# Kernel tuning notes

Measured on AMD Instinct MI355X. Metric: run time of the kernel, lower is better.

## Reference

```python
import jax, jax.numpy as jnp
import numpy as np

EPS = 1e-5
K_NBR = 21   # num_neighbors + 1 (self)
PSI = 4


def _bn(x, g, b):
    # BatchNorm (training-mode forward): channel-last, normalize over all other axes
    axes = tuple(range(x.ndim - 1))
    m = jnp.mean(x, axis=axes, keepdims=True)
    v = jnp.var(x, axis=axes, keepdims=True)
    return (x - m) * jax.lax.rsqrt(v + EPS) * g + b


def setup_inputs() -> dict:
    key = jax.random.key(0)
    ks = jax.random.split(key, 16)
    B, N, Cin, Cout = 4, 2048, 64, 256
    h = Cout // 2
    w_ch = Cout // PSI
    heads = 2 * PSI - 1

    def w(k, o, i):
        return jax.random.normal(k, (o, i), dtype=jnp.float32) * (1.0 / np.sqrt(i))

    p = {}
    p['xyz'] = jax.random.normal(ks[0], (B, N, 3), dtype=jnp.float32)
    p['f'] = jax.random.normal(ks[1], (B, Cin, N), dtype=jnp.float32)
    p['W_geo'] = w(ks[2], h, 6);       p['g_geo'] = jnp.ones(h);   p['b_geo'] = jnp.zeros(h)
    p['W_feat'] = w(ks[3], h, 2 * Cin); p['g_feat'] = jnp.ones(h); p['b_feat'] = jnp.zeros(h)
    p['g_bn'] = jnp.ones(Cout); p['b_bn'] = jnp.zeros(Cout)
    p['W_q'] = w(ks[4], Cout, Cout); p['g_q'] = jnp.ones(Cout); p['b_q'] = jnp.zeros(Cout)
    p['W_k'] = w(ks[5], Cout, Cout); p['g_k'] = jnp.ones(Cout); p['b_k'] = jnp.zeros(Cout)
    p['W_v'] = w(ks[6], Cout, Cout); p['g_v'] = jnp.ones(Cout); p['b_v'] = jnp.zeros(Cout)
    p['W_fus'] = w(ks[7], Cout, heads * w_ch); p['bias_fus'] = jnp.zeros(Cout)
    p['g_fus'] = jnp.ones(Cout); p['b_fus'] = jnp.zeros(Cout)
    p['g_ln'] = jnp.ones(Cout); p['b_ln'] = jnp.zeros(Cout)
    p['W_mlp'] = w(ks[8], Cout, Cout); p['bias_mlp'] = jnp.zeros(Cout)
    return p


def reference(xyz, f, W_geo, g_geo, b_geo, W_feat, g_feat, b_feat, g_bn, b_bn,
              W_q, g_q, b_q, W_k, g_k, b_k, W_v, g_v, b_v,
              W_fus, bias_fus, g_fus, b_fus, g_ln, b_ln, W_mlp, bias_mlp):
    B, N, _ = xyz.shape
    Cout = g_bn.shape[0]
    w_ch = Cout // PSI
    d_sh = w_ch // 2
    heads = 2 * PSI - 1

    # ---- PositionFusion: KNN grouping ----
    sq = jnp.sum(xyz * xyz, axis=-1)                                   # [B,N]
    d2 = sq[:, :, None] + sq[:, None, :] - 2.0 * jnp.einsum('bnd,bmd->bnm', xyz, xyz)
    _, idx = jax.lax.top_k(-d2, K_NBR)                                 # [B,N,K]

    grouped_xyz = jax.vmap(lambda p, i: p[i])(xyz, idx)                # [B,N,K,3]
    xyz_diff = grouped_xyz - xyz[:, :, None, :]
    geo_in = jnp.concatenate(
        [jnp.broadcast_to(xyz[:, :, None, :], grouped_xyz.shape), xyz_diff], axis=-1)  # [B,N,K,6]

    ft = jnp.transpose(f, (0, 2, 1))                                   # [B,N,Cin]
    grouped_f = jax.vmap(lambda p, i: p[i])(ft, idx)                   # [B,N,K,Cin]
    feat_in = jnp.concatenate(
        [grouped_f, jnp.broadcast_to(ft[:, :, None, :], grouped_f.shape)], axis=-1)    # [B,N,K,2Cin]

    geo = jax.nn.relu(_bn(jnp.einsum('bnki,oi->bnko', geo_in, W_geo), g_geo, b_geo))
    fea = jax.nn.relu(_bn(jnp.einsum('bnki,oi->bnko', feat_in, W_feat), g_feat, b_feat))
    feature_ = jnp.max(jnp.concatenate([geo, fea], axis=-1), axis=2)   # [B,N,Cout] (maxpool over K)

    # ---- BatchNorm1d ----
    x = _bn(feature_, g_bn, b_bn)

    # ---- Shifted-channel multi-head attention ----
    q = jax.nn.relu(_bn(jnp.einsum('bnc,oc->bno', x, W_q), g_q, b_q))
    k = jax.nn.relu(_bn(jnp.einsum('bnc,oc->bno', x, W_k), g_k, b_k))
    v = jax.nn.relu(_bn(jnp.einsum('bnc,oc->bno', x, W_v), g_v, b_v))

    qh = jnp.stack([q[..., m * d_sh:m * d_sh + w_ch] for m in range(heads)], axis=1)  # [B,H,N,w]
    kh = jnp.stack([k[..., m * d_sh:m * d_sh + w_ch] for m in range(heads)], axis=1)
    vh = jnp.stack([v[..., m * d_sh:m * d_sh + w_ch] for m in range(heads)], axis=1)

    a = jax.nn.softmax(jnp.einsum('bhnc,bhmc->bhnm', qh, kh), axis=-1)  # [B,H,N,N]
    o = jnp.einsum('bhnm,bhmc->bhnc', a, vh)                            # [B,H,N,w]
    O = jnp.transpose(o, (0, 2, 1, 3)).reshape(B, N, heads * w_ch)      # channel-concat per head

    fus = jax.nn.relu(_bn(jnp.einsum('bnc,oc->bno', O, W_fus) + bias_fus, g_fus, b_fus))

    feature__ = fus + feature_                                          # residual

    # ---- LayerNorm over channels ----
    m = jnp.mean(feature__, axis=-1, keepdims=True)
    var = jnp.var(feature__, axis=-1, keepdims=True)
    y = (feature__ - m) * jax.lax.rsqrt(var + EPS) * g_ln + b_ln

    out = feature__ + (jnp.einsum('bnc,oc->bno', y, W_mlp) + bias_mlp)
    return jnp.transpose(out, (0, 2, 1))                                # [B,Cout,N] like torch
```

## Files before the change

### kernel.cpp

```cpp
#include <hip/hip_runtime.h>
#include <math.h>

#define NB    4
#define NPTS  2048
#define ROWS  (NB*NPTS)
#define CIN   64
#define COUT  256
#define KNBR  21
#define NHEADS 7
#define WCH   64
#define DSH   32
#define LOG2E 1.4426950408889634f

typedef __attribute__((ext_vector_type(8))) short short8;
typedef __attribute__((ext_vector_type(4))) float floatx4;

#if __has_builtin(__builtin_amdgcn_exp2f)
#define EXP2(x) __builtin_amdgcn_exp2f(x)
#else
#define EXP2(x) __expf((x)*0.6931471805599453f)
#endif
#if __has_builtin(__builtin_amdgcn_rcpf)
#define RCP(x) __builtin_amdgcn_rcpf(x)
#else
#define RCP(x) (1.0f/(x))
#endif

__device__ __forceinline__ ushort f2bf(float x) {
    unsigned u = __float_as_uint(x);
    u += 0x7fffu + ((u >> 16) & 1u);
    return (ushort)(u >> 16);
}

template<int N>
__device__ __forceinline__ float dpp_ror16(float x) {
    return __int_as_float(__builtin_amdgcn_update_dpp(
        0, __float_as_int(x), 0x120 | N, 0xF, 0xF, true));
}
__device__ __forceinline__ float dpp_max16(float x) {
    x = fmaxf(x, dpp_ror16<1>(x));
    x = fmaxf(x, dpp_ror16<2>(x));
    x = fmaxf(x, dpp_ror16<4>(x));
    x = fmaxf(x, dpp_ror16<8>(x));
    return x;
}
__device__ __forceinline__ float dpp_sum16(float x) {
    x += dpp_ror16<1>(x);
    x += dpp_ror16<2>(x);
    x += dpp_ror16<4>(x);
    x += dpp_ror16<8>(x);
    return x;
}

template<int CTRL, int RMASK>
__device__ __forceinline__ unsigned dpp_umin_step(unsigned x) {
    unsigned t = (unsigned)__builtin_amdgcn_update_dpp((int)x, (int)x, CTRL, RMASK, 0xF, false);
    return (t < x) ? t : x;
}
__device__ __forceinline__ unsigned wave_min_u32(unsigned x) {
    x = dpp_umin_step<0x111, 0xF>(x);
    x = dpp_umin_step<0x112, 0xF>(x);
    x = dpp_umin_step<0x114, 0xF>(x);
    x = dpp_umin_step<0x118, 0xF>(x);
    x = dpp_umin_step<0x142, 0xA>(x);
    x = dpp_umin_step<0x143, 0xC>(x);
    return (unsigned)__builtin_amdgcn_readlane((int)x, 63);
}

__global__ __launch_bounds__(256) void prep_knn(const float* __restrict__ f, const float* __restrict__ Wf,
                                                const float* __restrict__ xyz, const float* __restrict__ Wg,
                                                const float* __restrict__ W_q, const float* __restrict__ W_k,
                                                const float* __restrict__ W_v, const float* __restrict__ W_fus,
                                                float* __restrict__ X, float* __restrict__ A,
                                                ushort* __restrict__ Wb, float* __restrict__ sums,
                                                int* __restrict__ idx) {
    __shared__ float4 SXQ[2048];
    int t = threadIdx.x;
    int blk = blockIdx.x;
    if (blk < 512) {
        float* As = (float*)SXQ;
        float* Ws = As + 16*68;
        int bx = blk & 127, by = blk >> 7;
        if (by == 0 && bx < 12) sums[bx*256 + t] = 0.f;
        int gid = (by*128 + bx)*256 + t;
        for (int i = gid; i < 311296; i += 131072) {
            const float* Wsrc; int off;
            if (i < 65536)       { Wsrc = W_q;   off = i; }
            else if (i < 131072) { Wsrc = W_k;   off = i - 65536; }
            else if (i < 196608) { Wsrc = W_v;   off = i - 131072; }
            else                 { Wsrc = W_fus; off = i - 196608; }
            Wb[i] = f2bf(Wsrc[off]);
        }
        int r0 = bx * 64, n0 = by * 64;
        for (int e = t; e < 4096; e += 256) {
            int row = r0 + (e >> 6), c = n0 + (e & 63), cc = c & 127;
            float x = xyz[row*3], y = xyz[row*3+1], z = xyz[row*3+2];
            const float* w = Wg + cc*6;
            float s = (c < 128) ? ((w[3]*x + w[4]*y) + w[5]*z)
                                : (((w[0]-w[3])*x + (w[1]-w[4])*y) + (w[2]-w[5])*z);
            A[(size_t)row*256 + c] = s;
        }
        int b = r0 >> 11, nbase = r0 & 2047;
        int tx = t & 15, ty = t >> 4;
        float acc[4][4];
#pragma unroll
        for (int i = 0; i < 4; i++)
#pragma unroll
            for (int j = 0; j < 4; j++) acc[i][j] = 0.f;
        int m64 = t & 63, kg = t >> 6;
        int lk = t & 15, lm = t >> 4;
        for (int k0 = 0; k0 < 64; k0 += 16) {
#pragma unroll
            for (int p = 0; p < 4; p++) {
                int k = kg*4 + p;
                As[k*68 + m64] = f[(size_t)b*CIN*NPTS + (size_t)(k0 + k)*NPTS + nbase + m64];
            }
#pragma unroll
            for (int i2 = 0; i2 < 4; i2++) {
                int cg = n0 + lm + 16*i2;
                Ws[lk*68 + lm + 16*i2] = Wf[(size_t)(cg & 127)*128 + (cg >> 7)*64 + k0 + lk];
            }
            __syncthreads();
#pragma unroll
            for (int kq = 0; kq < 16; kq++) {
                float4 a  = *(const float4*)&As[kq*68 + 4*ty];
                float4 b4 = *(const float4*)&Ws[kq*68 + 4*tx];
                float av[4] = {a.x, a.y, a.z, a.w};
                float bv[4] = {b4.x, b4.y, b4.z, b4.w};
#pragma unroll
                for (int i = 0; i < 4; i++)
#pragma unroll
                    for (int j = 0; j < 4; j++) acc[i][j] = fmaf(av[i], bv[j], acc[i][j]);
            }
            __syncthreads();
        }
#pragma unroll
        for (int i = 0; i < 4; i++)
#pragma unroll
            for (int j = 0; j < 4; j++)
                X[(size_t)(r0 + 4*ty + i)*256 + n0 + 4*tx + j] = acc[i][j];
        return;
    }
    int kb = blk - 512;
    int b = kb >> 9;
    int g = kb & 511;
    for (int m = t; m < NPTS; m += 256) {
        float x = xyz[(size_t)b*NPTS*3 + m*3];
        float y = xyz[(size_t)b*NPTS*3 + m*3 + 1];
        float z = xyz[(size_t)b*NPTS*3 + m*3 + 2];
        SXQ[m] = make_float4(x, y, z, (x*x + y*y) + z*z);
    }
    __syncthreads();
    int w = t >> 6, lane = t & 63;
    int n = g*4 + w;
    float4 q4 = SXQ[n];
    float qx = q4.x, qy = q4.y, qz = q4.z, sqn = q4.w;
    unsigned key[32];
#pragma unroll
    for (int i = 0; i < 32; i++) {
        int m = lane + (i << 6);
        float4 p = SXQ[m];
        float dt = (qx*p.x + qy*p.y) + qz*p.z;
        float d2 = fmaxf((sqn + p.w) - 2.0f*dt, 0.f);
        key[i] = (__float_as_uint(d2) & 0xFFFFF800u) | (unsigned)m;
    }
    unsigned winkey = 0xFFFFFFFFu;
    for (int kk = 0; kk < 32; kk++) {
        unsigned lv = key[0];
#pragma unroll
        for (int i = 1; i < 32; i++) lv = (key[i] < lv) ? key[i] : lv;
        unsigned win = wave_min_u32(lv);
        if (lane == kk) winkey = win;
        unsigned widx = win & 2047u;
        int slot = (int)(widx >> 6);
        bool own = (lane == (int)(widx & 63u));
#pragma unroll
        for (int i = 0; i < 32; i++)
            if (i == slot && own) key[i] = 0xFFFFFFFFu;
    }
    double d2r;
    int mr;
    {
        double qx64 = (double)qx, qy64 = (double)qy, qz64 = (double)qz;
        double sqn64 = qx64*qx64 + qy64*qy64 + qz64*qz64;
        if (lane < 32) {
            mr = (int)(winkey & 2047u);
            float4 p = SXQ[mr];
            double x = (double)p.x, y = (double)p.y, z = (double)p.z;
            double sqm = x*x + y*y + z*z;
            double dt  = qx64*x + qy64*y + qz64*z;
            d2r = (sqn64 + sqm) - 2.0*dt;
        } else {
            d2r = INFINITY; mr = 0x7FFFFFFF;
        }
    }
#pragma unroll
    for (int k = 2; k <= 32; k <<= 1) {
#pragma unroll
        for (int j = k >> 1; j > 0; j >>= 1) {
            double od = __shfl_xor(d2r, j, 64);
            int    om = __shfl_xor(mr, j, 64);
            bool up    = ((lane & k) == 0);
            bool lower = ((lane & j) == 0);
            bool oless = (od < d2r) || (od == d2r && om < mr);
            bool keepOther = up ? (lower ? oless : !oless) : (lower ? !oless : oless);
            if (keepOther) { d2r = od; mr = om; }
        }
    }
    if (lane < KNBR)
        idx[((size_t)b*NPTS + n)*KNBR + lane] = mr;
}

__global__ __launch_bounds__(256) void stats_gf(const float* __restrict__ geoBC, const float* __restrict__ featAC,
                                                const int* __restrict__ idx, const float* __restrict__ g_geo,
                                                const float* __restrict__ g_feat,
                                                float* __restrict__ sums, float* __restrict__ xsel) {
    int c = threadIdx.x;
    int cc = c & 127;
    const float* base = (c < 128) ? geoBC : featAC;
    bool wantmax = ((c < 128) ? g_geo[cc] : g_feat[cc]) >= 0.f;
    float s = 0.f, ss = 0.f;
    int r0 = blockIdx.x * 32;
    for (int r = r0; r < r0 + 32; r++) {
        int b = r >> 11;
        float ctr = base[(size_t)r*256 + 128 + cc];
        float mx = -1e30f, mn = 1e30f;
        const int* ip = idx + (size_t)r*KNBR;
        for (int kk = 0; kk < KNBR; kk++) {
            int j = ip[kk];
            float xv = ctr + base[((size_t)(b*NPTS + j))*256 + cc];
            mx = fmaxf(mx, xv); mn = fminf(mn, xv);
            s += xv; ss += xv*xv;
        }
        xsel[(size_t)r*256 + c] = wantmax ? mx : mn;
    }
    atomicAdd(&sums[c], s);
    atomicAdd(&sums[256 + c], ss);
}

__global__ __launch_bounds__(256) void feature_maxsel(const float* __restrict__ xsel, const float* __restrict__ sums,
                                                      const float* __restrict__ g_geo, const float* __restrict__ b_geo,
                                                      const float* __restrict__ g_feat, const float* __restrict__ b_feat,
                                                      float* __restrict__ feat, float* __restrict__ sums_bn1) {
    int c = threadIdx.x;
    const float inv = 1.0f / (float)(ROWS*KNBR);
    float mean = sums[c]*inv;
    float var  = sums[256+c]*inv - mean*mean;
    float g  = (c < 128) ? g_geo[c] : g_feat[c-128];
    float bb = (c < 128) ? b_geo[c] : b_feat[c-128];
    float sc = g / sqrtf(var + 1e-5f);
    float tt = bb - mean*sc;
    float s = 0.f, ss = 0.f;
    int r0 = blockIdx.x*32;
    for (int r = r0; r < r0+32; r++) {
        size_t i = (size_t)r*256 + c;
        float y = fmaxf(fmaf(sc, xsel[i], tt), 0.f);
        feat[i] = y; s += y; ss += y*y;
    }
    atomicAdd(&sums_bn1[c], s); atomicAdd(&sums_bn1[256+c], ss);
}

__global__ __launch_bounds__(256) void gemm_qkv(const float* __restrict__ Af, const float* __restrict__ sums_in,
                                                const float* __restrict__ g_bn, const float* __restrict__ b_bn,
                                                const ushort* __restrict__ Wb,
                                                float* __restrict__ QKVF, float* __restrict__ sums) {
    __shared__ float bns[2][256];
    __shared__ float red[4][256][2];
    int t = threadIdx.x;
    int r0 = blockIdx.x * 64, g = blockIdx.y;
    int w = t >> 6, lane = t & 63;
    int r15 = lane & 15, quad = lane >> 4;
    {
        float mean = sums_in[512 + t] * (1.0f/(float)ROWS);
        float var  = sums_in[768 + t] * (1.0f/(float)ROWS) - mean*mean;
        float sc = g_bn[t] / sqrtf(var + 1e-5f);
        bns[0][t] = sc;
        bns[1][t] = b_bn[t] - mean*sc;
    }
    __syncthreads();
    short8 aq[8];
    {
        const float* ap = Af + (size_t)(r0 + 16*w + r15)*256;
#pragma unroll
        for (int kc = 0; kc < 8; kc++) {
            int k0 = 32*kc + 8*quad;
            float4 a0 = *(const float4*)&ap[k0];
            float4 a1 = *(const float4*)&ap[k0+4];
            float4 s0 = *(const float4*)&bns[0][k0];
            float4 s1 = *(const float4*)&bns[0][k0+4];
            float4 h0 = *(const float4*)&bns[1][k0];
            float4 h1 = *(const float4*)&bns[1][k0+4];
            ushort u8[8];
            u8[0] = f2bf(fmaf(s0.x, a0.x, h0.x)); u8[1] = f2bf(fmaf(s0.y, a0.y, h0.y));
            u8[2] = f2bf(fmaf(s0.z, a0.z, h0.z)); u8[3] = f2bf(fmaf(s0.w, a0.w, h0.w));
            u8[4] = f2bf(fmaf(s1.x, a1.x, h1.x)); u8[5] = f2bf(fmaf(s1.y, a1.y, h1.y));
            u8[6] = f2bf(fmaf(s1.z, a1.z, h1.z)); u8[7] = f2bf(fmaf(s1.w, a1.w, h1.w));
            aq[kc] = *(short8*)u8;
        }
    }
    floatx4 zero4 = {0.f, 0.f, 0.f, 0.f};
    floatx4 acc[16];
#pragma unroll
    for (int st = 0; st < 16; st++) acc[st] = zero4;
    const ushort* wbase = Wb + (size_t)g*65536 + (size_t)r15*256 + 8*quad;
#pragma unroll
    for (int st = 0; st < 16; st++) {
        const ushort* wp = wbase + (size_t)(16*st)*256;
#pragma unroll
        for (int kc = 0; kc < 8; kc++) {
            short8 bf = *(const short8*)(wp + 32*kc);
            acc[st] = __builtin_amdgcn_mfma_f32_16x16x32_bf16(aq[kc], bf, acc[st], 0, 0, 0);
        }
    }
#pragma unroll
    for (int st = 0; st < 16; st++) {
        float s  = (acc[st][0] + acc[st][1]) + (acc[st][2] + acc[st][3]);
        float q2 = (acc[st][0]*acc[st][0] + acc[st][1]*acc[st][1]) +
                   (acc[st][2]*acc[st][2] + acc[st][3]*acc[st][3]);
        s  += __shfl_xor(s, 16, 64);  s  += __shfl_xor(s, 32, 64);
        q2 += __shfl_xor(q2, 16, 64); q2 += __shfl_xor(q2, 32, 64);
        if (lane < 16) { red[w][16*st + r15][0] = s; red[w][16*st + r15][1] = q2; }
#pragma unroll
        for (int reg = 0; reg < 4; reg++)
            QKVF[(size_t)(r0 + 16*w + 4*quad + reg)*768 + g*256 + 16*st + r15] = acc[st][reg];
    }
    __syncthreads();
    {
        float s = red[0][t][0] + red[1][t][0] + red[2][t][0] + red[3][t][0];
        float q = red[0][t][1] + red[1][t][1] + red[2][t][1] + red[3][t][1];
        atomicAdd(&sums[1024 + g*512 + t], s);
        atomicAdd(&sums[1024 + g*512 + 256 + t], q);
    }
}

__global__ __launch_bounds__(256) void affine_qkv(const float* __restrict__ QKVF, const float* __restrict__ sums,
                                                  const float* __restrict__ g_q, const float* __restrict__ b_q,
                                                  const float* __restrict__ g_k, const float* __restrict__ b_k,
                                                  const float* __restrict__ g_v, const float* __restrict__ b_v,
                                                  ushort* __restrict__ qk, ushort* __restrict__ vt) {
    __shared__ float sts[6][256];
    __shared__ ushort tile[64][72];
    int t = threadIdx.x;
    {
        const float* gs[3] = {g_q, g_k, g_v};
        const float* bs[3] = {b_q, b_k, b_v};
#pragma unroll
        for (int g = 0; g < 3; g++) {
            float mean = sums[1024 + g*512 + t] * (1.0f/(float)ROWS);
            float var  = sums[1024 + g*512 + 256 + t] * (1.0f/(float)ROWS) - mean*mean;
            float sc = gs[g][t] / sqrtf(var + 1e-5f);
            float sh = bs[g][t] - mean*sc;
            if (g == 0) { sc *= LOG2E; sh *= LOG2E; }
            sts[2*g][t] = sc;
            sts[2*g+1][t] = sh;
        }
    }
    __syncthreads();
    int r0 = blockIdx.x * 64, c0 = blockIdx.y * 64;
    int b = r0 >> 11, nbase = r0 & 2047;
    if (c0 < 512) {
#pragma unroll
        for (int rep = 0; rep < 16; rep++) {
            int e = t + 256*rep;
            int row = e >> 6, c = e & 63;
            int col = c0 + c, g = col >> 8, cc = col & 255;
            float v = QKVF[(size_t)(r0 + row)*768 + col];
            v = fmaxf(fmaf(sts[2*g][cc], v, sts[2*g+1][cc]), 0.f);
            qk[(size_t)(r0 + row)*512 + col] = f2bf(v);
        }
    } else {
#pragma unroll
        for (int rep = 0; rep < 16; rep++) {
            int e = t + 256*rep;
            int row = e >> 6, c = e & 63;
            int col = c0 + c, cc = col & 255;
            float v = QKVF[(size_t)(r0 + row)*768 + col];
            v = fmaxf(fmaf(sts[4][cc], v, sts[5][cc]), 0.f);
            tile[c][row] = f2bf(v);
        }
        __syncthreads();
#pragma unroll
        for (int rep = 0; rep < 16; rep++) {
            int e = t + 256*rep;
            int cc = e >> 6, nn = e & 63;
            vt[((size_t)(b*256 + (c0 - 512) + cc))*2048 + nbase + nn] = tile[cc][nn];
        }
    }
}

__global__ __launch_bounds__(512) void attn2(const ushort* __restrict__ qk, const ushort* __restrict__ vt,
                                             float* __restrict__ obuf) {
    __shared__ ushort Ksh[64*72];
    __shared__ ushort Vts[64*72];
    __shared__ ushort Psh[128*72];
    int h = blockIdx.y, b = blockIdx.z;
    int r0 = blockIdx.x * 128;
    int t = threadIdx.x;
    int w = t >> 6, lane = t & 63;
    int r15 = lane & 15, quad = lane >> 4;
    size_t rowbase = (size_t)b*NPTS;
    int hoff = h*DSH;

    short8 aq[2];
#pragma unroll
    for (int s = 0; s < 2; s++)
        aq[s] = *(const short8*)(qk + (rowbase + r0 + 16*w + r15)*512 + hoff + 32*s + 8*quad);

    floatx4 zero4 = {0.f, 0.f, 0.f, 0.f};
    floatx4 oacc[4];
    float mrun[4], lrun[4];
#pragma unroll
    for (int i = 0; i < 4; i++) { oacc[i] = zero4; mrun[i] = -1e30f; lrun[i] = 0.f; }

    for (int m0 = 0; m0 < NPTS; m0 += 64) {
        {
            int rr = t >> 3, c = t & 7;
            *(uint4*)&Ksh[rr*72 + 8*c] =
                *(const uint4*)(qk + (rowbase + m0 + rr)*512 + 256 + hoff + 8*c);
            *(uint4*)&Vts[rr*72 + 8*c] =
                *(const uint4*)(vt + ((size_t)(b*256 + hoff + rr))*2048 + m0 + 8*c);
        }
        __syncthreads();

        floatx4 sacc[4];
#pragma unroll
        for (int tt = 0; tt < 4; tt++) sacc[tt] = zero4;
#pragma unroll
        for (int tt = 0; tt < 4; tt++) {
            int key = 16*tt + r15;
#pragma unroll
            for (int s = 0; s < 2; s++) {
                short8 kf = *(const short8*)&Ksh[key*72 + 32*s + 8*quad];
                sacc[tt] = __builtin_amdgcn_mfma_f32_16x16x32_bf16(aq[s], kf, sacc[tt], 0, 0, 0);
            }
        }

        float pm[4][4];
#pragma unroll
        for (int reg = 0; reg < 4; reg++) {
            float rmax = fmaxf(fmaxf(sacc[0][reg], sacc[1][reg]),
                               fmaxf(sacc[2][reg], sacc[3][reg]));
            rmax = dpp_max16(rmax);
            float mnew = fmaxf(mrun[reg], rmax);
            float alpha = EXP2(mrun[reg] - mnew);
            float rs = 0.f;
#pragma unroll
            for (int tt = 0; tt < 4; tt++) {
                float p = EXP2(sacc[tt][reg] - mnew);
                pm[tt][reg] = p; rs += p;
            }
            rs = dpp_sum16(rs);
            lrun[reg] = lrun[reg]*alpha + rs;
            mrun[reg] = mnew;
#pragma unroll
            for (int td = 0; td < 4; td++) oacc[td][reg] *= alpha;
        }

#pragma unroll
        for (int reg = 0; reg < 4; reg++) {
            int row = 16*w + 4*quad + reg;
#pragma unroll
            for (int tt = 0; tt < 4; tt++)
                Psh[row*72 + 16*tt + r15] = f2bf(pm[tt][reg]);
        }

#pragma unroll
        for (int s = 0; s < 2; s++) {
            short8 pf = *(const short8*)&Psh[(16*w + r15)*72 + 32*s + 8*quad];
#pragma unroll
            for (int td = 0; td < 4; td++) {
                short8 vf = *(const short8*)&Vts[(16*td + r15)*72 + 32*s + 8*quad];
                oacc[td] = __builtin_amdgcn_mfma_f32_16x16x32_bf16(pf, vf, oacc[td], 0, 0, 0);
            }
        }
        __syncthreads();
    }

#pragma unroll
    for (int reg = 0; reg < 4; reg++) {
        int grow = r0 + 16*w + 4*quad + reg;
        float invl = RCP(lrun[reg]);
#pragma unroll
        for (int td = 0; td < 4; td++)
            obuf[(rowbase + grow)*(size_t)(NHEADS*WCH) + h*WCH + 16*td + r15] = oacc[td][reg]*invl;
    }
}

__global__ __launch_bounds__(256) void gemm_fus(const float* __restrict__ OBUF, const ushort* __restrict__ Wb,
                                                const float* __restrict__ bias, float* __restrict__ C,
                                                float* __restrict__ sums) {
    __shared__ float red[4][128][2];
    int t = threadIdx.x;
    int r0 = blockIdx.x * 64, n0 = blockIdx.y * 128;
    int w = t >> 6, lane = t & 63;
    int r15 = lane & 15, quad = lane >> 4;
    int arow = 16*w + r15;
    short8 aq[14];
    {
        const float* p0 = OBUF + (size_t)(r0 + arow)*448;
#pragma unroll
        for (int kc = 0; kc < 14; kc++) {
            int k0 = 32*kc + 8*quad;
            float4 x0 = *(const float4*)&p0[k0];
            float4 y0 = *(const float4*)&p0[k0+4];
            ushort u8[8];
            u8[0] = f2bf(x0.x); u8[1] = f2bf(x0.y);
            u8[2] = f2bf(x0.z); u8[3] = f2bf(x0.w);
            u8[4] = f2bf(y0.x); u8[5] = f2bf(y0.y);
            u8[6] = f2bf(y0.z); u8[7] = f2bf(y0.w);
            aq[kc] = *(short8*)u8;
        }
    }
    floatx4 zero4 = {0.f, 0.f, 0.f, 0.f};
    floatx4 acc[8];
#pragma unroll
    for (int st = 0; st < 8; st++) acc[st] = zero4;
    const ushort* wbase = Wb + 196608 + (size_t)(n0 + r15)*448 + 8*quad;
#pragma unroll
    for (int st = 0; st < 8; st++) {
        const ushort* wp = wbase + (size_t)(16*st)*448;
#pragma unroll
        for (int kc = 0; kc < 14; kc++) {
            short8 bf = *(const short8*)(wp + 32*kc);
            acc[st] = __builtin_amdgcn_mfma_f32_16x16x32_bf16(aq[kc], bf, acc[st], 0, 0, 0);
        }
    }
#pragma unroll
    for (int st = 0; st < 8; st++) {
        int col = n0 + 16*st + r15;
        float bi = bias[col];
        float v0 = acc[st][0] + bi, v1 = acc[st][1] + bi, v2 = acc[st][2] + bi, v3 = acc[st][3] + bi;
        float s  = (v0 + v1) + (v2 + v3);
        float q2 = (v0*v0 + v1*v1) + (v2*v2 + v3*v3);
        s  += __shfl_xor(s, 16, 64);  s  += __shfl_xor(s, 32, 64);
        q2 += __shfl_xor(q2, 16, 64); q2 += __shfl_xor(q2, 32, 64);
        if (lane < 16) { red[w][16*st + r15][0] = s; red[w][16*st + r15][1] = q2; }
        C[(size_t)(r0 + 16*w + 4*quad + 0)*256 + col] = v0;
        C[(size_t)(r0 + 16*w + 4*quad + 1)*256 + col] = v1;
        C[(size_t)(r0 + 16*w + 4*quad + 2)*256 + col] = v2;
        C[(size_t)(r0 + 16*w + 4*quad + 3)*256 + col] = v3;
    }
    __syncthreads();
    {
        int col = t >> 1, which = t & 1;
        float v = red[0][col][which] + red[1][col][which] + red[2][col][which] + red[3][col][which];
        atomicAdd(&sums[2560 + which*256 + n0 + col], v);
    }
}

__global__ __launch_bounds__(256) void gemm_mlp_ln(const float* __restrict__ FUSP, const float* __restrict__ A,
                                                   const float* __restrict__ sums,
                                                   const float* __restrict__ g_fus, const float* __restrict__ b_fus,
                                                   const float* __restrict__ g_ln, const float* __restrict__ b_ln,
                                                   const float* __restrict__ W, const float* __restrict__ bias,
                                                   float* __restrict__ outp) {
    __shared__ float Ys[256][68];
    __shared__ float FFs[64][65];
    __shared__ float Ws[16][68];
    __shared__ float tr[64][65];
    __shared__ float SC[256], SH[256], GL[256], BL[256];
    int t = threadIdx.x;
    int r0 = blockIdx.x*64, n0 = blockIdx.y*64;
    {
        float mean0 = sums[2560 + t] * (1.0f/(float)ROWS);
        float var0  = sums[2560 + 256 + t] * (1.0f/(float)ROWS) - mean0*mean0;
        float sc = g_fus[t] / sqrtf(var0 + 1e-5f);
        SC[t] = sc; SH[t] = b_fus[t] - mean0*sc;
        GL[t] = g_ln[t]; BL[t] = b_ln[t];
    }
    __syncthreads();
    int row = t >> 2, seg = t & 3;
    size_t rb = (size_t)(r0 + row)*256;
    float4 vv[16];
    float s = 0.f, ss = 0.f;
#pragma unroll
    for (int j = 0; j < 16; j++) {
        int c = seg*64 + 4*j;
        float4 fp = *(const float4*)&FUSP[rb + c];
        float4 fe = *(const float4*)&A[rb + c];
        float4 sc4 = *(const float4*)&SC[c];
        float4 sh4 = *(const float4*)&SH[c];
        float4 v;
        v.x = fmaxf(fmaf(sc4.x, fp.x, sh4.x), 0.f) + fe.x;
        v.y = fmaxf(fmaf(sc4.y, fp.y, sh4.y), 0.f) + fe.y;
        v.z = fmaxf(fmaf(sc4.z, fp.z, sh4.z), 0.f) + fe.z;
        v.w = fmaxf(fmaf(sc4.w, fp.w, sh4.w), 0.f) + fe.w;
        vv[j] = v;
        s  += (v.x + v.y) + (v.z + v.w);
        ss += (v.x*v.x + v.y*v.y) + (v.z*v.z + v.w*v.w);
        if (seg == blockIdx.y) *(float4*)&FFs[row][4*j] = v;
    }
    s  += __shfl_xor(s, 1, 64);  s  += __shfl_xor(s, 2, 64);
    ss += __shfl_xor(ss, 1, 64); ss += __shfl_xor(ss, 2, 64);
    float mean = s * (1.f/256.f);
    float var  = ss * (1.f/256.f) - mean*mean;
    float rin  = 1.f/sqrtf(var + 1e-5f);
#pragma unroll
    for (int j = 0; j < 16; j++) {
        int c = seg*64 + 4*j;
        float4 gl = *(const float4*)&GL[c];
        float4 bl = *(const float4*)&BL[c];
        float4 v = vv[j];
        Ys[c+0][row] = (v.x - mean)*rin*gl.x + bl.x;
        Ys[c+1][row] = (v.y - mean)*rin*gl.y + bl.y;
        Ys[c+2][row] = (v.z - mean)*rin*gl.z + bl.z;
        Ys[c+3][row] = (v.w - mean)*rin*gl.w + bl.w;
    }
    __syncthreads();
    int tx = t & 15, ty = t >> 4;
    int lk = t & 15, lm = t >> 4;
    float acc[4][4];
#pragma unroll
    for (int i = 0; i < 4; i++)
#pragma unroll
        for (int j = 0; j < 4; j++) acc[i][j] = 0.f;
    for (int k0 = 0; k0 < 256; k0 += 16) {
#pragma unroll
        for (int i2 = 0; i2 < 4; i2++)
            Ws[lk][lm + 16*i2] = W[(size_t)(n0 + lm + 16*i2)*256 + k0 + lk];
        __syncthreads();
#pragma unroll
        for (int kq = 0; kq < 16; kq++) {
            float4 a  = *(const float4*)&Ys[k0 + kq][4*ty];
            float4 b4 = *(const float4*)&Ws[kq][4*tx];
            float av[4] = {a.x, a.y, a.z, a.w};
            float bv[4] = {b4.x, b4.y, b4.z, b4.w};
#pragma unroll
            for (int i = 0; i < 4; i++)
#pragma unroll
                for (int j = 0; j < 4; j++) acc[i][j] = fmaf(av[i], bv[j], acc[i][j]);
        }
        __syncthreads();
    }
#pragma unroll
    for (int i = 0; i < 4; i++)
#pragma unroll
        for (int j = 0; j < 4; j++) {
            float v = acc[i][j] + bias[n0 + 4*tx + j] + FFs[4*ty + i][4*tx + j];
            tr[4*tx + j][4*ty + i] = v;
        }
    __syncthreads();
    int b = r0 >> 11, nbase = r0 & 2047;
#pragma unroll
    for (int rep = 0; rep < 16; rep++) {
        int e = t + 256*rep;
        int cl = e >> 6, nl = e & 63;
        outp[((size_t)(b*256 + n0 + cl))*2048 + nbase + nl] = tr[cl][nl];
    }
}

extern "C" void kernel_launch(void* const* d_in, const int* in_sizes, int n_in,
                              void* d_out, int out_size, void* d_ws, size_t ws_size,
                              hipStream_t stream) {
    const float* xyz    = (const float*)d_in[0];
    const float* f      = (const float*)d_in[1];
    const float* W_geo  = (const float*)d_in[2];
    const float* g_geo  = (const float*)d_in[3];
    const float* b_geo  = (const float*)d_in[4];
    const float* W_feat = (const float*)d_in[5];
    const float* g_feat = (const float*)d_in[6];
    const float* b_feat = (const float*)d_in[7];
    const float* g_bn   = (const float*)d_in[8];
    const float* b_bn   = (const float*)d_in[9];
    const float* W_q    = (const float*)d_in[10];
    const float* g_q    = (const float*)d_in[11];
    const float* b_q    = (const float*)d_in[12];
    const float* W_k    = (const float*)d_in[13];
    const float* g_k    = (const float*)d_in[14];
    const float* b_k    = (const float*)d_in[15];
    const float* W_v    = (const float*)d_in[16];
    const float* g_v    = (const float*)d_in[17];
    const float* b_v    = (const float*)d_in[18];
    const float* W_fus  = (const float*)d_in[19];
    const float* bias_fus = (const float*)d_in[20];
    const float* g_fus  = (const float*)d_in[21];
    const float* b_fus  = (const float*)d_in[22];
    const float* g_ln   = (const float*)d_in[23];
    const float* b_ln   = (const float*)d_in[24];
    const float* W_mlp  = (const float*)d_in[25];
    const float* bias_mlp = (const float*)d_in[26];

    float* ws = (float*)d_ws;
    const size_t MBF = 262144;
    float* SUMS  = ws;
    int*   IDX   = (int*)(ws + 16384);
    float* A     = ws + 1*MBF;
    float* X     = ws + 9*MBF;
    ushort* QK16 = (ushort*)(ws + 9*MBF);
    float* FUSP  = ws + 9*MBF;
    float* CSEL  = ws + 17*MBF;
    float* QKVF  = ws + 17*MBF;
    float* OBUF  = ws + 17*MBF;
    ushort* VT16 = (ushort*)(ws + 45*MBF);
    ushort* WB16 = (ushort*)(ws + 49*MBF);

    prep_knn<<<2560, 256, 0, stream>>>(f, W_feat, xyz, W_geo, W_q, W_k, W_v, W_fus,
                                       X, A, WB16, SUMS, IDX);
    stats_gf<<<256, 256, 0, stream>>>(A, X, IDX, g_geo, g_feat, SUMS, CSEL);
    feature_maxsel<<<256, 256, 0, stream>>>(CSEL, SUMS, g_geo, b_geo, g_feat, b_feat, A, SUMS + 512);
    gemm_qkv<<<dim3(128, 3), 256, 0, stream>>>(A, SUMS, g_bn, b_bn, WB16, QKVF, SUMS);
    affine_qkv<<<dim3(128, 12), 256, 0, stream>>>(QKVF, SUMS, g_q, b_q, g_k, b_k, g_v, b_v, QK16, VT16);
    attn2<<<dim3(NPTS/128, NHEADS, NB), 512, 0, stream>>>(QK16, VT16, OBUF);
    gemm_fus<<<dim3(128, 2), 256, 0, stream>>>(OBUF, WB16, bias_fus, FUSP, SUMS);
    gemm_mlp_ln<<<dim3(128, 4), 256, 0, stream>>>(FUSP, A, SUMS, g_fus, b_fus, g_ln, b_ln,
                                                  W_mlp, bias_mlp, (float*)d_out);
}
```

Measured before the change: 421.1 us.

## Transpose attention MFMA so each lane owns one query row

Swaps the MFMA operand order in the attention kernel so each lane holds one query row's scores. The online softmax then needs only two cross-lane shuffles for max and sum instead of DPP reductions over 16-lane rows, and keeps one running max and sum per lane. It adds a wave-uniform skip of the rescale when no row's max grows, packs P to bf16 with v_cvt_pk_bf16_f32 and 8-byte LDS stores, and writes the output as float4. Packed bf16 conversion may round differently from the old manual rounding.

New measurement: 396.0 us. -6.0%, faster.

```diff
diff --git a/kernel.cpp b/kernel.cpp
--- a/kernel.cpp
+++ b/kernel.cpp
@@ -32,24 +32,10 @@
     return (ushort)(u >> 16);
 }
 
-template<int N>
-__device__ __forceinline__ float dpp_ror16(float x) {
-    return __int_as_float(__builtin_amdgcn_update_dpp(
-        0, __float_as_int(x), 0x120 | N, 0xF, 0xF, true));
-}
-__device__ __forceinline__ float dpp_max16(float x) {
-    x = fmaxf(x, dpp_ror16<1>(x));
-    x = fmaxf(x, dpp_ror16<2>(x));
-    x = fmaxf(x, dpp_ror16<4>(x));
-    x = fmaxf(x, dpp_ror16<8>(x));
-    return x;
-}
-__device__ __forceinline__ float dpp_sum16(float x) {
-    x += dpp_ror16<1>(x);
-    x += dpp_ror16<2>(x);
-    x += dpp_ror16<4>(x);
-    x += dpp_ror16<8>(x);
-    return x;
+__device__ __forceinline__ unsigned cvt_pk_bf16(float lo, float hi) {
+    unsigned r;
+    asm("v_cvt_pk_bf16_f32 %0, %1, %2" : "=v"(r) : "v"(lo), "v"(hi));
+    return r;
 }
 
 template<int CTRL, int RMASK>
@@ -408,9 +394,11 @@
 
     floatx4 zero4 = {0.f, 0.f, 0.f, 0.f};
     floatx4 oacc[4];
-    float mrun[4], lrun[4];
-#pragma unroll
-    for (int i = 0; i < 4; i++) { oacc[i] = zero4; mrun[i] = -1e30f; lrun[i] = 0.f; }
+    float mrun = -1e30f, lrun = 0.f;
+#pragma unroll
+    for (int i = 0; i < 4; i++) oacc[i] = zero4;
+
+    ushort* prow = &Psh[(16*w + r15)*72];
 
     for (int m0 = 0; m0 < NPTS; m0 += 64) {
         {
@@ -431,58 +419,62 @@
 #pragma unroll
             for (int s = 0; s < 2; s++) {
                 short8 kf = *(const short8*)&Ksh[key*72 + 32*s + 8*quad];
-                sacc[tt] = __builtin_amdgcn_mfma_f32_16x16x32_bf16(aq[s], kf, sacc[tt], 0, 0, 0);
+                sacc[tt] = __builtin_amdgcn_mfma_f32_16x16x32_bf16(kf, aq[s], sacc[tt], 0, 0, 0);
             }
         }
 
-        float pm[4][4];
-#pragma unroll
-        for (int reg = 0; reg < 4; reg++) {
-            float rmax = fmaxf(fmaxf(sacc[0][reg], sacc[1][reg]),
-                               fmaxf(sacc[2][reg], sacc[3][reg]));
-            rmax = dpp_max16(rmax);
-            float mnew = fmaxf(mrun[reg], rmax);
-            float alpha = EXP2(mrun[reg] - mnew);
-            float rs = 0.f;
-#pragma unroll
-            for (int tt = 0; tt < 4; tt++) {
-                float p = EXP2(sacc[tt][reg] - mnew);
-                pm[tt][reg] = p; rs += p;
-            }
-            rs = dpp_sum16(rs);
-            lrun[reg] = lrun[reg]*alpha + rs;
-            mrun[reg] = mnew;
-#pragma unroll
-            for (int td = 0; td < 4; td++) oacc[td][reg] *= alpha;
-        }
-
-#pragma unroll
-        for (int reg = 0; reg < 4; reg++) {
-            int row = 16*w + 4*quad + reg;
-#pragma unroll
-            for (int tt = 0; tt < 4; tt++)
-                Psh[row*72 + 16*tt + r15] = f2bf(pm[tt][reg]);
-        }
+        float mx = sacc[0][0];
+#pragma unroll
+        for (int tt = 0; tt < 4; tt++)
+#pragma unroll
+            for (int reg = 0; reg < 4; reg++) mx = fmaxf(mx, sacc[tt][reg]);
+        mx = fmaxf(mx, __shfl_xor(mx, 16, 64));
+        mx = fmaxf(mx, __shfl_xor(mx, 32, 64));
+
+        if (!__all(mx <= mrun)) {
+            float mnew = fmaxf(mrun, mx);
+            float alpha = EXP2(mrun - mnew);
+            lrun *= alpha;
+#pragma unroll
+            for (int td = 0; td < 4; td++) oacc[td] *= alpha;
+            mrun = mnew;
+        }
+
+        float rs = 0.f;
+#pragma unroll
+        for (int tt = 0; tt < 4; tt++) {
+            float p0 = EXP2(sacc[tt][0] - mrun);
+            float p1 = EXP2(sacc[tt][1] - mrun);
+            float p2 = EXP2(sacc[tt][2] - mrun);
+            float p3 = EXP2(sacc[tt][3] - mrun);
+            rs += (p0 + p1) + (p2 + p3);
+            uint2 pk2;
+            pk2.x = cvt_pk_bf16(p0, p1);
+            pk2.y = cvt_pk_bf16(p2, p3);
+            *(uint2*)&prow[16*tt + 4*quad] = pk2;
+        }
+        rs += __shfl_xor(rs, 16, 64);
+        rs += __shfl_xor(rs, 32, 64);
+        lrun += rs;
 
 #pragma unroll
         for (int s = 0; s < 2; s++) {
-            short8 pf = *(const short8*)&Psh[(16*w + r15)*72 + 32*s + 8*quad];
+            short8 pf = *(const short8*)&prow[32*s + 8*quad];
 #pragma unroll
             for (int td = 0; td < 4; td++) {
                 short8 vf = *(const short8*)&Vts[(16*td + r15)*72 + 32*s + 8*quad];
-                oacc[td] = __builtin_amdgcn_mfma_f32_16x16x32_bf16(pf, vf, oacc[td], 0, 0, 0);
+                oacc[td] = __builtin_amdgcn_mfma_f32_16x16x32_bf16(vf, pf, oacc[td], 0, 0, 0);
             }
         }
         __syncthreads();
     }
 
-#pragma unroll
-    for (int reg = 0; reg < 4; reg++) {
-        int grow = r0 + 16*w + 4*quad + reg;
-        float invl = RCP(lrun[reg]);
-#pragma unroll
-        for (int td = 0; td < 4; td++)
-            obuf[(rowbase + grow)*(size_t)(NHEADS*WCH) + h*WCH + 16*td + r15] = oacc[td][reg]*invl;
+    float invl = RCP(lrun);
+#pragma unroll
+    for (int td = 0; td < 4; td++) {
+        floatx4 o = oacc[td] * invl;
+        *(float4*)&obuf[(rowbase + r0 + 16*w + r15)*(size_t)(NHEADS*WCH) + h*WCH + 16*td + 4*quad] =
+            *(float4*)&o;
     }
 }
 
```
